# Optimization experiments

Hardware: AMD Instinct MI355X
Metric: run time of the kernel (lower is better)

The kernel has to match this reference:

```python
import jax, jax.numpy as jnp
import numpy as np

N_NODES = 50000
N_EDGES = 800000
D = 128


def setup_inputs() -> dict:
    key = jax.random.key(0)
    k1, k2, k3, k4, k5 = jax.random.split(key, 5)
    node_attr = jax.random.normal(k1, (N_NODES, D), dtype=jnp.float32)
    edge_index = jax.random.randint(k2, (2, N_EDGES), 0, N_NODES, dtype=jnp.int64)
    edge_attr = jax.random.normal(k3, (N_EDGES, D), dtype=jnp.float32)
    # 2-layer MLP: (3D -> D) -> ReLU -> (D -> D), scaled init
    w1 = jax.random.normal(k4, (3 * D, D), dtype=jnp.float32) * (1.0 / np.sqrt(3 * D))
    b1 = jnp.zeros((D,), dtype=jnp.float32)
    w2 = jax.random.normal(k5, (D, D), dtype=jnp.float32) * (1.0 / np.sqrt(D))
    b2 = jnp.zeros((D,), dtype=jnp.float32)
    return {"node_attr": node_attr, "edge_index": edge_index, "edge_attr": edge_attr,
            "w1": w1, "b1": b1, "w2": w2, "b2": b2}


def reference(node_attr, edge_index, edge_attr, w1, b1, w2, b2):
    senders_idx = edge_index[0]
    receivers_idx = edge_index[1]
    senders_attr = node_attr[senders_idx]      # [E, D] irregular gather
    receivers_attr = node_attr[receivers_idx]  # [E, D] irregular gather
    collected = jnp.concatenate([senders_attr, receivers_attr, edge_attr], axis=1)  # [E, 3D]
    h = jax.nn.relu(collected @ w1 + b1)       # [E, D]
    edge_attr_new = h @ w2 + b2                # [E, D]
    return edge_attr_new
```

## Files before the change

### kernel.cpp

```cpp
#include <hip/hip_runtime.h>


#define NE 800000
#define DD 128

typedef float f32x4v __attribute__((ext_vector_type(4)));
typedef float f32x16 __attribute__((ext_vector_type(16)));
typedef _Float16 f16x8 __attribute__((ext_vector_type(8)));
typedef _Float16 f16x4 __attribute__((ext_vector_type(4)));

__device__ __forceinline__ f16x4 cvt4(f32x4v v) {
    f16x4 r;
    r[0] = (_Float16)v[0]; r[1] = (_Float16)v[1];
    r[2] = (_Float16)v[2]; r[3] = (_Float16)v[3];
    return r;
}

__global__ void prep_w(const float* __restrict__ w1, const float* __restrict__ w2,
                       _Float16* __restrict__ w1t, _Float16* __restrict__ w2f) {
    int i = blockIdx.x * 256 + threadIdx.x;
    if (i < 384 * 128) {
        int col = i / 384;
        int k = i - col * 384;
        float v = w1[(size_t)k * 128 + col];
        int byteoff = col * 768 + ((k * 2) ^ ((col & 15) << 4));
        *(_Float16*)((char*)w1t + byteoff) = (_Float16)v;
    } else {
        int j = i - 384 * 128;
        int kk2 = j >> 10;
        int col = (j >> 3) & 127;
        int jj = j & 7;
        w2f[j] = (_Float16)w2[(size_t)(kk2 * 8 + jj) * 128 + col];
    }
}

__global__ __attribute__((amdgpu_flat_work_group_size(512, 512),
                          amdgpu_waves_per_eu(2, 2)))
void edge_mlp(
    const float* __restrict__ node_attr,
    const int* __restrict__ eidx,
    const float* __restrict__ edge_attr,
    const _Float16* __restrict__ w1t,
    const float* __restrict__ b1,
    const _Float16* __restrict__ w2f,
    const float* __restrict__ b2,
    float* __restrict__ out) {
    extern __shared__ char lds[];

    const int tid = threadIdx.x;
    const int wid = tid >> 6;
    const int lane = tid & 63;
    const int r31 = lane & 31;
    const int g2 = lane >> 5;
    const int sub = lane >> 5;
    const int c4 = lane & 31;

    {
        const char* src = (const char*)w1t;
        #pragma unroll
        for (int i = 0; i < 12; i++) {
            int off = (tid + i * 512) * 16;
            *(f16x8*)(lds + off) = *(const f16x8*)(src + off);
        }
    }

    float b1v[4], b2v[4];
    #pragma unroll
    for (int n = 0; n < 4; n++) { b1v[n] = b1[n * 32 + r31]; b2v[n] = b2[n * 32 + r31]; }

    __syncthreads();

    char* ab = lds + 96 * 1024 + wid * 8192;
    const int ebase = blockIdx.x * 256 + wid * 32;

    const int sidx = eidx[ebase + r31];
    const int ridx = eidx[NE + ebase + r31];

    f32x4v sv[16];
    #pragma unroll
    for (int i = 0; i < 16; i++) {
        int r = __shfl(sidx, 2 * i + sub);
        sv[i] = *(const f32x4v*)(node_attr + (size_t)r * DD + c4 * 4);
    }
    #pragma unroll
    for (int i = 0; i < 16; i++) {
        const int row = 2 * i + sub;
        *(f16x4*)(ab + row * 256 + ((c4 * 8) ^ ((row & 15) << 4))) = cvt4(sv[i]);
    }

    f32x4v rv[16];
    #pragma unroll
    for (int i = 0; i < 16; i++) {
        int r = __shfl(ridx, 2 * i + sub);
        rv[i] = *(const f32x4v*)(node_attr + (size_t)r * DD + c4 * 4);
    }

    f32x16 acc[4] = {};
    const int xa = (r31 & 15) << 4;

    #pragma unroll
    for (int kk8 = 0; kk8 < 8; kk8++) {
        f16x8 a = *(const f16x8*)(ab + r31 * 256 + ((kk8 * 32 + g2 * 16) ^ xa));
        #pragma unroll
        for (int n = 0; n < 4; n++) {
            const int col = n * 32 + r31;
            f16x8 b = *(const f16x8*)(lds + col * 768 + (((0 * 8 + kk8) * 32 + g2 * 16) ^ ((col & 15) << 4)));
            acc[n] = __builtin_amdgcn_mfma_f32_32x32x16_f16(a, b, acc[n], 0, 0, 0);
        }
    }

    #pragma unroll
    for (int i = 0; i < 16; i++) {
        const int row = 2 * i + sub;
        *(f16x4*)(ab + row * 256 + ((c4 * 8) ^ ((row & 15) << 4))) = cvt4(rv[i]);
    }
    f32x4v ev[16];
    #pragma unroll
    for (int i = 0; i < 16; i++) {
        const int row = 2 * i + sub;
        ev[i] = __builtin_nontemporal_load(
            (const f32x4v*)(edge_attr + (size_t)(ebase + row) * DD + c4 * 4));
    }

    #pragma unroll
    for (int kk8 = 0; kk8 < 8; kk8++) {
        f16x8 a = *(const f16x8*)(ab + r31 * 256 + ((kk8 * 32 + g2 * 16) ^ xa));
        #pragma unroll
        for (int n = 0; n < 4; n++) {
            const int col = n * 32 + r31;
            f16x8 b = *(const f16x8*)(lds + col * 768 + (((1 * 8 + kk8) * 32 + g2 * 16) ^ ((col & 15) << 4)));
            acc[n] = __builtin_amdgcn_mfma_f32_32x32x16_f16(a, b, acc[n], 0, 0, 0);
        }
    }

    #pragma unroll
    for (int i = 0; i < 16; i++) {
        const int row = 2 * i + sub;
        *(f16x4*)(ab + row * 256 + ((c4 * 8) ^ ((row & 15) << 4))) = cvt4(ev[i]);
    }

    f16x8 b2fa[4][4];
    #pragma unroll
    for (int kk = 0; kk < 4; kk++)
        #pragma unroll
        for (int n = 0; n < 4; n++)
            b2fa[kk][n] = *(const f16x8*)(w2f + ((size_t)(kk * 2 + g2) * 128 + n * 32 + r31) * 8);

    #pragma unroll
    for (int kk8 = 0; kk8 < 8; kk8++) {
        f16x8 a = *(const f16x8*)(ab + r31 * 256 + ((kk8 * 32 + g2 * 16) ^ xa));
        #pragma unroll
        for (int n = 0; n < 4; n++) {
            const int col = n * 32 + r31;
            f16x8 b = *(const f16x8*)(lds + col * 768 + (((2 * 8 + kk8) * 32 + g2 * 16) ^ ((col & 15) << 4)));
            acc[n] = __builtin_amdgcn_mfma_f32_32x32x16_f16(a, b, acc[n], 0, 0, 0);
        }
    }

    #pragma unroll
    for (int n = 0; n < 4; n++) {
        const int col = n * 32 + r31;
        #pragma unroll
        for (int reg = 0; reg < 16; reg++) {
            const int row = (reg & 3) + 8 * (reg >> 2) + 4 * g2;
            float v = fmaxf(acc[n][reg] + b1v[n], 0.0f);
            *(_Float16*)(ab + row * 256 + ((col * 2) ^ ((row & 15) << 4))) = (_Float16)v;
        }
    }

    f32x16 acc2[4] = {};
    #pragma unroll
    for (int kk = 0; kk < 4; kk++) {
        f16x8 a = *(const f16x8*)(ab + r31 * 256 + ((kk * 32 + g2 * 16) ^ xa));
        #pragma unroll
        for (int n = 0; n < 4; n++)
            acc2[n] = __builtin_amdgcn_mfma_f32_32x32x16_f16(a, b2fa[kk][n], acc2[n], 0, 0, 0);
    }
    f16x8 b2fb[4][4];
    #pragma unroll
    for (int kk = 0; kk < 4; kk++)
        #pragma unroll
        for (int n = 0; n < 4; n++)
            b2fb[kk][n] = *(const f16x8*)(w2f + ((size_t)((kk + 4) * 2 + g2) * 128 + n * 32 + r31) * 8);
    #pragma unroll
    for (int kk = 4; kk < 8; kk++) {
        f16x8 a = *(const f16x8*)(ab + r31 * 256 + ((kk * 32 + g2 * 16) ^ xa));
        #pragma unroll
        for (int n = 0; n < 4; n++)
            acc2[n] = __builtin_amdgcn_mfma_f32_32x32x16_f16(a, b2fb[kk - 4][n], acc2[n], 0, 0, 0);
    }

    #pragma unroll
    for (int n = 0; n < 4; n++) {
        #pragma unroll
        for (int reg = 0; reg < 16; reg++) {
            const int row = (reg & 3) + 8 * (reg >> 2) + 4 * g2;
            __builtin_nontemporal_store(acc2[n][reg] + b2v[n],
                out + (size_t)(ebase + row) * DD + n * 32 + r31);
        }
    }
}

extern "C" void kernel_launch(void* const* d_in, const int* in_sizes, int n_in,
                              void* d_out, int out_size, void* d_ws, size_t ws_size,
                              hipStream_t stream) {
    const float* node_attr = (const float*)d_in[0];
    const int* eidx = (const int*)d_in[1];
    const float* edge_attr = (const float*)d_in[2];
    const float* w1 = (const float*)d_in[3];
    const float* b1 = (const float*)d_in[4];
    const float* w2 = (const float*)d_in[5];
    const float* b2 = (const float*)d_in[6];
    float* out = (float*)d_out;

    _Float16* w1t = (_Float16*)d_ws;
    _Float16* w2f = w1t + 384 * 128;

    hipFuncSetAttribute((const void*)edge_mlp,
                        hipFuncAttributeMaxDynamicSharedMemorySize, 160 * 1024);

    prep_w<<<256, 256, 0, stream>>>(w1, w2, w1t, w2f);
    edge_mlp<<<3125, 512, 160 * 1024, stream>>>(node_attr, eidx, edge_attr,
                                                w1t, b1, w2f, b2, out);
}
```

Before: 272.6 us.

## Stream W1 fragments from global memory instead of LDS to raise occupancy

W1 is no longer staged into a 96KB LDS copy per block. Each wave now loads pre-packed fp16 W1 MMA fragments directly from global/L2, and LDS holds only a small per-wave activation buffer. Blocks shrink to 256 threads with more waves per EU, and all three gathers (sender, receiver, edge) are issued up front to overlap latency. The trade-off is more global/L2 traffic for weight fragments and higher register pressure from holding 48 prefetched vectors.

```diff
diff --git a/kernel.cpp b/kernel.cpp
--- a/kernel.cpp
+++ b/kernel.cpp
@@ -17,66 +17,54 @@
 }
 
 __global__ void prep_w(const float* __restrict__ w1, const float* __restrict__ w2,
-                       _Float16* __restrict__ w1t, _Float16* __restrict__ w2f) {
+                       _Float16* __restrict__ w1f, _Float16* __restrict__ w2f) {
     int i = blockIdx.x * 256 + threadIdx.x;
-    if (i < 384 * 128) {
-        int col = i / 384;
-        int k = i - col * 384;
-        float v = w1[(size_t)k * 128 + col];
-        int byteoff = col * 768 + ((k * 2) ^ ((col & 15) << 4));
-        *(_Float16*)((char*)w1t + byteoff) = (_Float16)v;
+    if (i < 48 * 128 * 8) {
+        int kk2 = i >> 10;
+        int col = (i >> 3) & 127;
+        int j = i & 7;
+        w1f[i] = (_Float16)w1[(size_t)(kk2 * 8 + j) * 128 + col];
     } else {
-        int j = i - 384 * 128;
-        int kk2 = j >> 10;
-        int col = (j >> 3) & 127;
-        int jj = j & 7;
-        w2f[j] = (_Float16)w2[(size_t)(kk2 * 8 + jj) * 128 + col];
-    }
-}
-
-__global__ __attribute__((amdgpu_flat_work_group_size(512, 512),
-                          amdgpu_waves_per_eu(2, 2)))
+        int t = i - 48 * 128 * 8;
+        int kk2 = t >> 10;
+        int col = (t >> 3) & 127;
+        int j = t & 7;
+        w2f[t] = (_Float16)w2[(size_t)(kk2 * 8 + j) * 128 + col];
+    }
+}
+
+__global__ __attribute__((amdgpu_flat_work_group_size(256, 256),
+                          amdgpu_waves_per_eu(5, 5)))
 void edge_mlp(
     const float* __restrict__ node_attr,
     const int* __restrict__ eidx,
     const float* __restrict__ edge_attr,
-    const _Float16* __restrict__ w1t,
+    const _Float16* __restrict__ w1f,
     const float* __restrict__ b1,
     const _Float16* __restrict__ w2f,
     const float* __restrict__ b2,
     float* __restrict__ out) {
-    extern __shared__ char lds[];
+    __shared__ _Float16 abuf[4][4096];
 
     const int tid = threadIdx.x;
     const int wid = tid >> 6;
     const int lane = tid & 63;
     const int r31 = lane & 31;
     const int g2 = lane >> 5;
-    const int sub = lane >> 5;
-    const int c4 = lane & 31;
-
-    {
-        const char* src = (const char*)w1t;
-        #pragma unroll
-        for (int i = 0; i < 12; i++) {
-            int off = (tid + i * 512) * 16;
-            *(f16x8*)(lds + off) = *(const f16x8*)(src + off);
-        }
-    }
-
-    float b1v[4], b2v[4];
-    #pragma unroll
-    for (int n = 0; n < 4; n++) { b1v[n] = b1[n * 32 + r31]; b2v[n] = b2[n * 32 + r31]; }
-
-    __syncthreads();
-
-    char* ab = lds + 96 * 1024 + wid * 8192;
-    const int ebase = blockIdx.x * 256 + wid * 32;
+    const int sub = g2;
+    const int c4 = r31;
+
+    char* ab = (char*)abuf[wid];
+    const int ebase = blockIdx.x * 128 + wid * 32;
 
     const int sidx = eidx[ebase + r31];
     const int ridx = eidx[NE + ebase + r31];
 
-    f32x4v sv[16];
+    float b1v[4], b2v[4];
+    #pragma unroll
+    for (int n = 0; n < 4; n++) { b1v[n] = b1[n * 32 + r31]; b2v[n] = b2[n * 32 + r31]; }
+
+    f32x4v sv[16], rv[16], ev[16];
     #pragma unroll
     for (int i = 0; i < 16; i++) {
         int r = __shfl(sidx, 2 * i + sub);
@@ -84,27 +72,33 @@
     }
     #pragma unroll
     for (int i = 0; i < 16; i++) {
-        const int row = 2 * i + sub;
-        *(f16x4*)(ab + row * 256 + ((c4 * 8) ^ ((row & 15) << 4))) = cvt4(sv[i]);
-    }
-
-    f32x4v rv[16];
-    #pragma unroll
-    for (int i = 0; i < 16; i++) {
         int r = __shfl(ridx, 2 * i + sub);
         rv[i] = *(const f32x4v*)(node_attr + (size_t)r * DD + c4 * 4);
     }
+    #pragma unroll
+    for (int i = 0; i < 16; i++) {
+        const int row = 2 * i + sub;
+        ev[i] = __builtin_nontemporal_load(
+            (const f32x4v*)(edge_attr + (size_t)(ebase + row) * DD + c4 * 4));
+    }
+
+    const int xa = (r31 & 15) << 4;
 
     f32x16 acc[4] = {};
-    const int xa = (r31 & 15) << 4;
-
+
+    #pragma unroll
+    for (int i = 0; i < 16; i++) {
+        const int row = 2 * i + sub;
+        *(f16x4*)(ab + row * 256 + ((c4 * 8) ^ ((row & 15) << 4))) = cvt4(sv[i]);
+    }
+    __builtin_amdgcn_wave_barrier();
     #pragma unroll
     for (int kk8 = 0; kk8 < 8; kk8++) {
         f16x8 a = *(const f16x8*)(ab + r31 * 256 + ((kk8 * 32 + g2 * 16) ^ xa));
+        const int kk = 0 * 8 + kk8;
         #pragma unroll
         for (int n = 0; n < 4; n++) {
-            const int col = n * 32 + r31;
-            f16x8 b = *(const f16x8*)(lds + col * 768 + (((0 * 8 + kk8) * 32 + g2 * 16) ^ ((col & 15) << 4)));
+            f16x8 b = *(const f16x8*)(w1f + ((size_t)((kk * 2 + g2) * 128 + n * 32 + r31)) * 8);
             acc[n] = __builtin_amdgcn_mfma_f32_32x32x16_f16(a, b, acc[n], 0, 0, 0);
         }
     }
@@ -114,21 +108,14 @@
         const int row = 2 * i + sub;
         *(f16x4*)(ab + row * 256 + ((c4 * 8) ^ ((row & 15) << 4))) = cvt4(rv[i]);
     }
-    f32x4v ev[16];
-    #pragma unroll
-    for (int i = 0; i < 16; i++) {
-        const int row = 2 * i + sub;
-        ev[i] = __builtin_nontemporal_load(
-            (const f32x4v*)(edge_attr + (size_t)(ebase + row) * DD + c4 * 4));
-    }
-
+    __builtin_amdgcn_wave_barrier();
     #pragma unroll
     for (int kk8 = 0; kk8 < 8; kk8++) {
         f16x8 a = *(const f16x8*)(ab + r31 * 256 + ((kk8 * 32 + g2 * 16) ^ xa));
+        const int kk = 1 * 8 + kk8;
         #pragma unroll
         for (int n = 0; n < 4; n++) {
-            const int col = n * 32 + r31;
-            f16x8 b = *(const f16x8*)(lds + col * 768 + (((1 * 8 + kk8) * 32 + g2 * 16) ^ ((col & 15) << 4)));
+            f16x8 b = *(const f16x8*)(w1f + ((size_t)((kk * 2 + g2) * 128 + n * 32 + r31)) * 8);
             acc[n] = __builtin_amdgcn_mfma_f32_32x32x16_f16(a, b, acc[n], 0, 0, 0);
         }
     }
@@ -138,21 +125,20 @@
         const int row = 2 * i + sub;
         *(f16x4*)(ab + row * 256 + ((c4 * 8) ^ ((row & 15) << 4))) = cvt4(ev[i]);
     }
-
     f16x8 b2fa[4][4];
     #pragma unroll
     for (int kk = 0; kk < 4; kk++)
         #pragma unroll
         for (int n = 0; n < 4; n++)
-            b2fa[kk][n] = *(const f16x8*)(w2f + ((size_t)(kk * 2 + g2) * 128 + n * 32 + r31) * 8);
-
+            b2fa[kk][n] = *(const f16x8*)(w2f + ((size_t)((kk * 2 + g2) * 128 + n * 32 + r31)) * 8);
+    __builtin_amdgcn_wave_barrier();
     #pragma unroll
     for (int kk8 = 0; kk8 < 8; kk8++) {
         f16x8 a = *(const f16x8*)(ab + r31 * 256 + ((kk8 * 32 + g2 * 16) ^ xa));
+        const int kk = 2 * 8 + kk8;
         #pragma unroll
         for (int n = 0; n < 4; n++) {
-            const int col = n * 32 + r31;
-            f16x8 b = *(const f16x8*)(lds + col * 768 + (((2 * 8 + kk8) * 32 + g2 * 16) ^ ((col & 15) << 4)));
+            f16x8 b = *(const f16x8*)(w1f + ((size_t)((kk * 2 + g2) * 128 + n * 32 + r31)) * 8);
             acc[n] = __builtin_amdgcn_mfma_f32_32x32x16_f16(a, b, acc[n], 0, 0, 0);
         }
     }
@@ -167,6 +153,7 @@
             *(_Float16*)(ab + row * 256 + ((col * 2) ^ ((row & 15) << 4))) = (_Float16)v;
         }
     }
+    __builtin_amdgcn_wave_barrier();
 
     f32x16 acc2[4] = {};
     #pragma unroll
@@ -181,7 +168,7 @@
     for (int kk = 0; kk < 4; kk++)
         #pragma unroll
         for (int n = 0; n < 4; n++)
-            b2fb[kk][n] = *(const f16x8*)(w2f + ((size_t)((kk + 4) * 2 + g2) * 128 + n * 32 + r31) * 8);
+            b2fb[kk][n] = *(const f16x8*)(w2f + ((size_t)(((kk + 4) * 2 + g2) * 128 + n * 32 + r31)) * 8);
     #pragma unroll
     for (int kk = 4; kk < 8; kk++) {
         f16x8 a = *(const f16x8*)(ab + r31 * 256 + ((kk * 32 + g2 * 16) ^ xa));
@@ -213,13 +200,10 @@
     const float* b2 = (const float*)d_in[6];
     float* out = (float*)d_out;
 
-    _Float16* w1t = (_Float16*)d_ws;
-    _Float16* w2f = w1t + 384 * 128;
-
-    hipFuncSetAttribute((const void*)edge_mlp,
-                        hipFuncAttributeMaxDynamicSharedMemorySize, 160 * 1024);
-
-    prep_w<<<256, 256, 0, stream>>>(w1, w2, w1t, w2f);
-    edge_mlp<<<3125, 512, 160 * 1024, stream>>>(node_attr, eidx, edge_attr,
-                                                w1t, b1, w2f, b2, out);
-}
+    _Float16* w1f = (_Float16*)d_ws;
+    _Float16* w2f = w1f + 48 * 128 * 8;
+
+    prep_w<<<256, 256, 0, stream>>>(w1, w2, w1f, w2f);
+    edge_mlp<<<6250, 256, 0, stream>>>(node_attr, eidx, edge_attr,
+                                       w1f, b1, w2f, b2, out);
+}
```

Measured after the change: 899.2 us. 3.3x slower.

## Process two edge tiles per wave and prefetch next tile's gather during MLP

Applied to the files above, without the earlier changes.

Each wave now handles two 32-edge tiles instead of one, halving the grid and amortizing the 96KB W1 LDS preload and W2 register load across twice the work. The sender gather for the second tile is issued before the first tile's second GEMM and output stores so its latency overlaps compute. Sched barriers and wave barriers pin the instruction order. It keeps all 32 W2 fragments live in registers, which raises register pressure at the fixed two waves per EU and could cause spills.

```diff
diff --git a/kernel.cpp b/kernel.cpp
--- a/kernel.cpp
+++ b/kernel.cpp
@@ -34,6 +34,26 @@
     }
 }
 
+#define MFMA_SEG(SEG)                                                                     \
+    _Pragma("unroll")                                                                     \
+    for (int kk8 = 0; kk8 < 8; kk8++) {                                                   \
+        f16x8 a = *(const f16x8*)(ab + r31 * 256 + ((kk8 * 32 + g2 * 16) ^ xa));          \
+        _Pragma("unroll")                                                                 \
+        for (int n = 0; n < 4; n++) {                                                     \
+            const int col = n * 32 + r31;                                                 \
+            f16x8 b = *(const f16x8*)(lds + col * 768 +                                   \
+                       ((((SEG) * 8 + kk8) * 32 + g2 * 16) ^ ((col & 15) << 4)));         \
+            acc[n] = __builtin_amdgcn_mfma_f32_32x32x16_f16(a, b, acc[n], 0, 0, 0);       \
+        }                                                                                 \
+    }
+
+#define WRITE_SEG(V)                                                                      \
+    _Pragma("unroll")                                                                     \
+    for (int i = 0; i < 16; i++) {                                                        \
+        const int row = 2 * i + g2;                                                       \
+        *(f16x4*)(ab + row * 256 + ((r31 * 8) ^ ((row & 15) << 4))) = cvt4(V[i]);         \
+    }
+
 __global__ __attribute__((amdgpu_flat_work_group_size(512, 512),
                           amdgpu_waves_per_eu(2, 2)))
 void edge_mlp(
@@ -52,8 +72,6 @@
     const int lane = tid & 63;
     const int r31 = lane & 31;
     const int g2 = lane >> 5;
-    const int sub = lane >> 5;
-    const int c4 = lane & 31;
 
     {
         const char* src = (const char*)w1t;
@@ -70,92 +88,66 @@
 
     __syncthreads();
 
+    const int ebase0 = blockIdx.x * 512 + wid * 64;
+    if (ebase0 >= NE) return;
+    const int ebase1 = ebase0 + 32;
+
     char* ab = lds + 96 * 1024 + wid * 8192;
-    const int ebase = blockIdx.x * 256 + wid * 32;
-
-    const int sidx = eidx[ebase + r31];
-    const int ridx = eidx[NE + ebase + r31];
-
-    f32x4v sv[16];
-    #pragma unroll
-    for (int i = 0; i < 16; i++) {
-        int r = __shfl(sidx, 2 * i + sub);
-        sv[i] = *(const f32x4v*)(node_attr + (size_t)r * DD + c4 * 4);
-    }
-    #pragma unroll
-    for (int i = 0; i < 16; i++) {
-        const int row = 2 * i + sub;
-        *(f16x4*)(ab + row * 256 + ((c4 * 8) ^ ((row & 15) << 4))) = cvt4(sv[i]);
-    }
-
-    f32x4v rv[16];
-    #pragma unroll
-    for (int i = 0; i < 16; i++) {
-        int r = __shfl(ridx, 2 * i + sub);
-        rv[i] = *(const f32x4v*)(node_attr + (size_t)r * DD + c4 * 4);
-    }
+    const int xa = (r31 & 15) << 4;
+
+    const int sidx0 = eidx[ebase0 + r31];
+    const int ridx0 = eidx[NE + ebase0 + r31];
+    const int sidx1 = eidx[ebase1 + r31];
+    const int ridx1 = eidx[NE + ebase1 + r31];
+
+    f16x8 b2f[8][4];
+    #pragma unroll
+    for (int kk = 0; kk < 8; kk++)
+        #pragma unroll
+        for (int n = 0; n < 4; n++)
+            b2f[kk][n] = *(const f16x8*)(w2f + ((size_t)((kk * 2 + g2) * 128 + n * 32 + r31)) * 8);
+
+    f32x4v sv[16], rv[16], ev[16];
+    #pragma unroll
+    for (int i = 0; i < 16; i++) {
+        int r = __shfl(sidx0, 2 * i + g2);
+        sv[i] = *(const f32x4v*)(node_attr + (size_t)r * DD + r31 * 4);
+    }
+    __builtin_amdgcn_sched_barrier(0);
+    WRITE_SEG(sv)
+    #pragma unroll
+    for (int i = 0; i < 16; i++) {
+        int r = __shfl(ridx0, 2 * i + g2);
+        rv[i] = *(const f32x4v*)(node_attr + (size_t)r * DD + r31 * 4);
+    }
+    __builtin_amdgcn_sched_barrier(0);
 
     f32x16 acc[4] = {};
-    const int xa = (r31 & 15) << 4;
-
-    #pragma unroll
-    for (int kk8 = 0; kk8 < 8; kk8++) {
-        f16x8 a = *(const f16x8*)(ab + r31 * 256 + ((kk8 * 32 + g2 * 16) ^ xa));
-        #pragma unroll
-        for (int n = 0; n < 4; n++) {
-            const int col = n * 32 + r31;
-            f16x8 b = *(const f16x8*)(lds + col * 768 + (((0 * 8 + kk8) * 32 + g2 * 16) ^ ((col & 15) << 4)));
-            acc[n] = __builtin_amdgcn_mfma_f32_32x32x16_f16(a, b, acc[n], 0, 0, 0);
-        }
-    }
-
-    #pragma unroll
-    for (int i = 0; i < 16; i++) {
-        const int row = 2 * i + sub;
-        *(f16x4*)(ab + row * 256 + ((c4 * 8) ^ ((row & 15) << 4))) = cvt4(rv[i]);
-    }
-    f32x4v ev[16];
-    #pragma unroll
-    for (int i = 0; i < 16; i++) {
-        const int row = 2 * i + sub;
+    __builtin_amdgcn_wave_barrier();
+    MFMA_SEG(0)
+
+    WRITE_SEG(rv)
+    #pragma unroll
+    for (int i = 0; i < 16; i++) {
+        const int row = 2 * i + g2;
         ev[i] = __builtin_nontemporal_load(
-            (const f32x4v*)(edge_attr + (size_t)(ebase + row) * DD + c4 * 4));
-    }
-
-    #pragma unroll
-    for (int kk8 = 0; kk8 < 8; kk8++) {
-        f16x8 a = *(const f16x8*)(ab + r31 * 256 + ((kk8 * 32 + g2 * 16) ^ xa));
-        #pragma unroll
-        for (int n = 0; n < 4; n++) {
-            const int col = n * 32 + r31;
-            f16x8 b = *(const f16x8*)(lds + col * 768 + (((1 * 8 + kk8) * 32 + g2 * 16) ^ ((col & 15) << 4)));
-            acc[n] = __builtin_amdgcn_mfma_f32_32x32x16_f16(a, b, acc[n], 0, 0, 0);
-        }
-    }
-
-    #pragma unroll
-    for (int i = 0; i < 16; i++) {
-        const int row = 2 * i + sub;
-        *(f16x4*)(ab + row * 256 + ((c4 * 8) ^ ((row & 15) << 4))) = cvt4(ev[i]);
-    }
-
-    f16x8 b2fa[4][4];
-    #pragma unroll
-    for (int kk = 0; kk < 4; kk++)
-        #pragma unroll
-        for (int n = 0; n < 4; n++)
-            b2fa[kk][n] = *(const f16x8*)(w2f + ((size_t)(kk * 2 + g2) * 128 + n * 32 + r31) * 8);
-
-    #pragma unroll
-    for (int kk8 = 0; kk8 < 8; kk8++) {
-        f16x8 a = *(const f16x8*)(ab + r31 * 256 + ((kk8 * 32 + g2 * 16) ^ xa));
-        #pragma unroll
-        for (int n = 0; n < 4; n++) {
-            const int col = n * 32 + r31;
-            f16x8 b = *(const f16x8*)(lds + col * 768 + (((2 * 8 + kk8) * 32 + g2 * 16) ^ ((col & 15) << 4)));
-            acc[n] = __builtin_amdgcn_mfma_f32_32x32x16_f16(a, b, acc[n], 0, 0, 0);
-        }
-    }
+            (const f32x4v*)(edge_attr + (size_t)(ebase0 + row) * DD + r31 * 4));
+    }
+    __builtin_amdgcn_sched_barrier(0);
+    __builtin_amdgcn_wave_barrier();
+    MFMA_SEG(1)
+
+    WRITE_SEG(ev)
+    __builtin_amdgcn_wave_barrier();
+    MFMA_SEG(2)
+
+    f32x4v sv1[16];
+    #pragma unroll
+    for (int i = 0; i < 16; i++) {
+        int r = __shfl(sidx1, 2 * i + g2);
+        sv1[i] = *(const f32x4v*)(node_attr + (size_t)r * DD + r31 * 4);
+    }
+    __builtin_amdgcn_sched_barrier(0);
 
     #pragma unroll
     for (int n = 0; n < 4; n++) {
@@ -167,37 +159,85 @@
             *(_Float16*)(ab + row * 256 + ((col * 2) ^ ((row & 15) << 4))) = (_Float16)v;
         }
     }
-
-    f32x16 acc2[4] = {};
-    #pragma unroll
-    for (int kk = 0; kk < 4; kk++) {
-        f16x8 a = *(const f16x8*)(ab + r31 * 256 + ((kk * 32 + g2 * 16) ^ xa));
+    __builtin_amdgcn_wave_barrier();
+
+    {
+        f32x16 acc2[4] = {};
+        #pragma unroll
+        for (int kk = 0; kk < 8; kk++) {
+            f16x8 a = *(const f16x8*)(ab + r31 * 256 + ((kk * 32 + g2 * 16) ^ xa));
+            #pragma unroll
+            for (int n = 0; n < 4; n++)
+                acc2[n] = __builtin_amdgcn_mfma_f32_32x32x16_f16(a, b2f[kk][n], acc2[n], 0, 0, 0);
+        }
         #pragma unroll
         for (int n = 0; n < 4; n++)
-            acc2[n] = __builtin_amdgcn_mfma_f32_32x32x16_f16(a, b2fa[kk][n], acc2[n], 0, 0, 0);
-    }
-    f16x8 b2fb[4][4];
-    #pragma unroll
-    for (int kk = 0; kk < 4; kk++)
-        #pragma unroll
-        for (int n = 0; n < 4; n++)
-            b2fb[kk][n] = *(const f16x8*)(w2f + ((size_t)((kk + 4) * 2 + g2) * 128 + n * 32 + r31) * 8);
-    #pragma unroll
-    for (int kk = 4; kk < 8; kk++) {
-        f16x8 a = *(const f16x8*)(ab + r31 * 256 + ((kk * 32 + g2 * 16) ^ xa));
-        #pragma unroll
-        for (int n = 0; n < 4; n++)
-            acc2[n] = __builtin_amdgcn_mfma_f32_32x32x16_f16(a, b2fb[kk - 4][n], acc2[n], 0, 0, 0);
-    }
+            #pragma unroll
+            for (int reg = 0; reg < 16; reg++) {
+                const int row = (reg & 3) + 8 * (reg >> 2) + 4 * g2;
+                __builtin_nontemporal_store(acc2[n][reg] + b2v[n],
+                    out + (size_t)(ebase0 + row) * DD + n * 32 + r31);
+            }
+    }
+
+    __builtin_amdgcn_wave_barrier();
+    WRITE_SEG(sv1)
+    #pragma unroll
+    for (int i = 0; i < 16; i++) {
+        int r = __shfl(ridx1, 2 * i + g2);
+        rv[i] = *(const f32x4v*)(node_attr + (size_t)r * DD + r31 * 4);
+    }
+    __builtin_amdgcn_sched_barrier(0);
+
+    #pragma unroll
+    for (int n = 0; n < 4; n++) acc[n] = (f32x16)(0.0f);
+    __builtin_amdgcn_wave_barrier();
+    MFMA_SEG(0)
+
+    WRITE_SEG(rv)
+    #pragma unroll
+    for (int i = 0; i < 16; i++) {
+        const int row = 2 * i + g2;
+        ev[i] = __builtin_nontemporal_load(
+            (const f32x4v*)(edge_attr + (size_t)(ebase1 + row) * DD + r31 * 4));
+    }
+    __builtin_amdgcn_sched_barrier(0);
+    __builtin_amdgcn_wave_barrier();
+    MFMA_SEG(1)
+
+    WRITE_SEG(ev)
+    __builtin_amdgcn_wave_barrier();
+    MFMA_SEG(2)
 
     #pragma unroll
     for (int n = 0; n < 4; n++) {
+        const int col = n * 32 + r31;
         #pragma unroll
         for (int reg = 0; reg < 16; reg++) {
             const int row = (reg & 3) + 8 * (reg >> 2) + 4 * g2;
-            __builtin_nontemporal_store(acc2[n][reg] + b2v[n],
-                out + (size_t)(ebase + row) * DD + n * 32 + r31);
-        }
+            float v = fmaxf(acc[n][reg] + b1v[n], 0.0f);
+            *(_Float16*)(ab + row * 256 + ((col * 2) ^ ((row & 15) << 4))) = (_Float16)v;
+        }
+    }
+    __builtin_amdgcn_wave_barrier();
+
+    {
+        f32x16 acc2[4] = {};
+        #pragma unroll
+        for (int kk = 0; kk < 8; kk++) {
+            f16x8 a = *(const f16x8*)(ab + r31 * 256 + ((kk * 32 + g2 * 16) ^ xa));
+            #pragma unroll
+            for (int n = 0; n < 4; n++)
+                acc2[n] = __builtin_amdgcn_mfma_f32_32x32x16_f16(a, b2f[kk][n], acc2[n], 0, 0, 0);
+        }
+        #pragma unroll
+        for (int n = 0; n < 4; n++)
+            #pragma unroll
+            for (int reg = 0; reg < 16; reg++) {
+                const int row = (reg & 3) + 8 * (reg >> 2) + 4 * g2;
+                __builtin_nontemporal_store(acc2[n][reg] + b2v[n],
+                    out + (size_t)(ebase1 + row) * DD + n * 32 + r31);
+            }
     }
 }
 
@@ -220,6 +260,6 @@
                         hipFuncAttributeMaxDynamicSharedMemorySize, 160 * 1024);
 
     prep_w<<<256, 256, 0, stream>>>(w1, w2, w1t, w2f);
-    edge_mlp<<<3125, 512, 160 * 1024, stream>>>(node_attr, eidx, edge_attr,
+    edge_mlp<<<1563, 512, 160 * 1024, stream>>>(node_attr, eidx, edge_attr,
                                                 w1t, b1, w2f, b2, out);
 }
```

Result: slower. 648.6 us (+137.9%).
